# Kernel tuning notes

Hardware: AMD Instinct MI355X
Metric: run time of the kernel (lower is better)

## Reference

```python
import jax, jax.numpy as jnp
import numpy as np

K = 1024   # number of NNLS components (theta_1 is K x K)
B = 8192   # batched frames / columns


def setup_inputs() -> dict:
    key = jax.random.key(0)
    k1, k2, k3, k4 = jax.random.split(key, 4)
    # theta_1 = I - AtA / ||AtA||_F  -> near-identity contraction; emulate with
    # identity minus a small random symmetric-ish perturbation.
    pert = jax.random.normal(k1, (K, K), dtype=jnp.float32) * (1.0 / K)
    th1 = jnp.eye(K, dtype=jnp.float32) - pert
    Y = jax.random.uniform(k2, (K, B), dtype=jnp.float32)
    X_old = jax.random.uniform(k3, (K, B), dtype=jnp.float32)
    weight = jax.random.normal(k4, (K, B), dtype=jnp.float32) * 0.1  # theta_2 = Atb/n_AtA
    k = 2  # PGD iteration counter
    return {"th1": th1, "Y": Y, "X_old": X_old, "k": k, "weight": weight}


def reference(th1, Y, X_old, k, weight):
    # One projected-gradient-descent step of NNLS with Nesterov momentum:
    #   new_X = relu(th1 @ Y + weight)
    #   Y_new = new_X + (k-1)/(k+2) * (new_X - X_old)
    kf = jnp.float32(k)
    new_X = jax.nn.relu(jnp.matmul(th1, Y) + weight)          # [K, B]
    momentum = (kf - 1.0) / (kf + 2.0)
    Y_new = new_X + momentum * (new_X - X_old)                # [K, B]
    return (Y_new, new_X, k + 1, weight)
```

## Files before the change

### kernel.cpp

```cpp
#include <hip/hip_runtime.h>
#include <cstdint>


#define KDIM 1024
#define NDIM 8192
#define KB_ELEMS (1024UL * 8192UL)
#define YT_BYTES (8192UL * 1024UL * 2UL)
#define AB_BYTES (1024UL * 1024UL * 2UL)
#define WS_NEED (YT_BYTES + AB_BYTES)

typedef short short8 __attribute__((ext_vector_type(8)));
typedef float f32x4 __attribute__((ext_vector_type(4)));

struct __attribute__((aligned(4))) f4u { float x, y, z, w; };

__device__ __forceinline__ uint32_t pk2(float a, float b) {
  uint32_t ua = __builtin_bit_cast(uint32_t, a) + 0x8000u;
  uint32_t ub = __builtin_bit_cast(uint32_t, b) + 0x8000u;
  return (ua >> 16) | (ub & 0xFFFF0000u);
}

__device__ __forceinline__ void ldsload16(const void* g, void* l) {
  __builtin_amdgcn_global_load_lds(
      (const __attribute__((address_space(1))) uint32_t*)g,
      (__attribute__((address_space(3))) uint32_t*)l, 16, 0, 0);
}

__global__ __launch_bounds__(256) void nnls_conv(
    const float* __restrict__ th1, const float* __restrict__ Y,
    char* __restrict__ ws)
{
  unsigned short* yt  = (unsigned short*)ws;
  unsigned short* abf = (unsigned short*)(ws + YT_BYTES);
  const int tid = threadIdx.x;
  if (blockIdx.x < 1024) {
    const int kt = blockIdx.x >> 5;
    const int n  = (blockIdx.x & 31) * 256 + tid;
    const float* src = Y + (size_t)kt * 32 * NDIM + n;
    float v[32];
#pragma unroll
    for (int r = 0; r < 32; ++r) v[r] = src[(size_t)r * NDIM];
    __attribute__((aligned(16))) uint32_t o[16];
#pragma unroll
    for (int r = 0; r < 16; ++r) o[r] = pk2(v[2 * r], v[2 * r + 1]);
    const int perm = (n >> 1) & 3;
    uint4* dst = (uint4*)(yt + ((size_t)kt * NDIM + n) * 32);
    const uint4* o4 = (const uint4*)o;
#pragma unroll
    for (int q = 0; q < 4; ++q) dst[q ^ perm] = o4[q];
  } else {
    const int id = (blockIdx.x - 1024) * 256 + tid;
    const int kt = id >> 10, m = id & 1023;
    const float4* s4 = (const float4*)(th1 + (size_t)m * KDIM + kt * 32);
    __attribute__((aligned(16))) uint32_t o[16];
#pragma unroll
    for (int q = 0; q < 8; ++q) {
      const float4 v = s4[q];
      o[2 * q]     = pk2(v.x, v.y);
      o[2 * q + 1] = pk2(v.z, v.w);
    }
    const int perm = (m >> 1) & 3;
    uint4* dst = (uint4*)(abf + ((size_t)kt * KDIM + m) * 32);
    const uint4* o4 = (const uint4*)o;
#pragma unroll
    for (int q = 0; q < 4; ++q) dst[q ^ perm] = o4[q];
  }
}

__global__ __launch_bounds__(128, 2) void nnls_gemm3(
    const char* __restrict__ ws, const float* __restrict__ xold,
    const int* __restrict__ kin, const float* __restrict__ weight,
    float* __restrict__ out)
{
  const char* yt = ws;
  const char* ab = ws + YT_BYTES;
  __shared__ __align__(16) char smem[24576];

  const int tid  = threadIdx.x;
  const int lane = tid & 63;
  const int w    = tid >> 6;
  const int quad = lane >> 4, nl = lane & 15;

  const int m0 = blockIdx.y * 128;
  const int n0 = blockIdx.x * 64;

  const char* ag = ab + (size_t)m0 * 64 + w * 4096 + lane * 16;
  const char* bg = yt + (size_t)n0 * 64 + w * 2048 + lane * 16;

  f32x4 acc[4][4] = {};

  {
#pragma unroll
    for (int q = 0; q < 4; ++q) ldsload16(ag + q * 1024, smem + w * 4096 + q * 1024);
#pragma unroll
    for (int q = 0; q < 2; ++q) ldsload16(bg + q * 1024, smem + 8192 + w * 2048 + q * 1024);
  }
  __syncthreads();

  const int fro = (quad ^ ((nl >> 1) & 3)) * 8;

#pragma unroll 2
  for (int kt = 0; kt < 32; ++kt) {
    char* cur = smem + (kt & 1) * 12288;
    char* nxt = smem + ((kt & 1) ^ 1) * 12288;
    if (kt < 31) {
      const char* a2 = ag + (size_t)(kt + 1) * 65536;
      const char* b2 = bg + (size_t)(kt + 1) * 524288;
#pragma unroll
      for (int q = 0; q < 4; ++q) ldsload16(a2 + q * 1024, nxt + w * 4096 + q * 1024);
#pragma unroll
      for (int q = 0; q < 2; ++q) ldsload16(b2 + q * 1024, nxt + 8192 + w * 2048 + q * 1024);
    }
    const unsigned short* Asp = (const unsigned short*)cur;
    const unsigned short* Bsp = (const unsigned short*)(cur + 8192);
    short8 af[4], bf[4];
#pragma unroll
    for (int i = 0; i < 4; ++i)
      af[i] = *(const short8*)&Asp[(w * 64 + i * 16 + nl) * 32 + fro];
#pragma unroll
    for (int j = 0; j < 4; ++j)
      bf[j] = *(const short8*)&Bsp[(j * 16 + nl) * 32 + fro];
#pragma unroll
    for (int i = 0; i < 4; ++i)
#pragma unroll
      for (int j = 0; j < 4; ++j)
        acc[i][j] = __builtin_amdgcn_mfma_f32_16x16x32_bf16(af[i], bf[j], acc[i][j], 0, 0, 0);
    __syncthreads();
  }

  const float kf  = (float)kin[0];
  const float mom = (kf - 1.0f) / (kf + 2.0f);
  float* ep = (float*)(smem + w * 4608);
  const int u  = lane >> 4;
  const int cq = lane & 15;

#pragma unroll
  for (int i = 0; i < 4; ++i) {
    const int mgb = m0 + w * 64 + i * 16;
    size_t idxs[4]; float4 wv[4], xo[4];
#pragma unroll
    for (int t = 0; t < 4; ++t) {
      idxs[t] = (size_t)(mgb + t * 4 + u) * NDIM + n0 + cq * 4;
      wv[t] = *(const float4*)&weight[idxs[t]];
      xo[t] = *(const float4*)&xold[idxs[t]];
    }
#pragma unroll
    for (int j = 0; j < 4; ++j)
#pragma unroll
      for (int r = 0; r < 4; ++r)
        ep[(quad * 4 + r) * 68 + j * 16 + nl] = acc[i][j][r];
#pragma unroll
    for (int t = 0; t < 4; ++t) {
      const float4 cv = *(const float4*)&ep[(t * 4 + u) * 68 + cq * 4];
      const size_t idx = idxs[t];
      float4 nx, yn;
      nx.x = fmaxf(cv.x + wv[t].x, 0.0f); nx.y = fmaxf(cv.y + wv[t].y, 0.0f);
      nx.z = fmaxf(cv.z + wv[t].z, 0.0f); nx.w = fmaxf(cv.w + wv[t].w, 0.0f);
      yn.x = nx.x + mom * (nx.x - xo[t].x); yn.y = nx.y + mom * (nx.y - xo[t].y);
      yn.z = nx.z + mom * (nx.z - xo[t].z); yn.w = nx.w + mom * (nx.w - xo[t].w);
      *(float4*)&out[idx] = yn;
      *(float4*)&out[KB_ELEMS + idx] = nx;
      f4u s; s.x = wv[t].x; s.y = wv[t].y; s.z = wv[t].z; s.w = wv[t].w;
      *(f4u*)&out[2 * KB_ELEMS + 1 + idx] = s;
    }
  }

  if (blockIdx.x == 0 && blockIdx.y == 0 && tid == 0)
    out[2 * KB_ELEMS] = (float)(kin[0] + 1);
}

#define LDA 40
__global__ __launch_bounds__(512, 4) void nnls_gemm_v1(
    const float* __restrict__ th1, const float* __restrict__ Y,
    const float* __restrict__ xold, const int* __restrict__ kin,
    const float* __restrict__ weight, float* __restrict__ out)
{
  __shared__ __align__(16) char smem[40960];
  unsigned short* As0 = (unsigned short*)smem;
  unsigned short* Bs0 = (unsigned short*)(smem + 10240);
  unsigned short* As1 = (unsigned short*)(smem + 20480);
  unsigned short* Bs1 = (unsigned short*)(smem + 30720);

  const int tid  = threadIdx.x;
  const int lane = tid & 63;
  const int w    = tid >> 6;
  const int wm = w >> 1, wn = w & 1;
  const int quad = lane >> 4, nl = lane & 15;
  const int m0 = blockIdx.y * 128;
  const int n0 = blockIdx.x * 128;
  const int ar = tid >> 3;
  const int ac = tid & 7;
  const float* abase = th1 + (size_t)(m0 + ar) * KDIM + ac * 4;
  const int bn = tid & 127;
  const int bk = (tid >> 7) * 8;
  const float* ybase = Y + (size_t)bk * NDIM + n0 + bn;

  float4 abv[2];
  float  yb[8];
  abv[0] = *(const float4*)(abase);
  abv[1] = *(const float4*)(abase + (size_t)64 * KDIM);
#pragma unroll
  for (int r = 0; r < 8; ++r) yb[r] = ybase[(size_t)r * NDIM];

  f32x4 acc[2][4] = {};

#pragma unroll 2
  for (int kt = 0; kt < 32; ++kt) {
    unsigned short* Asp = (kt & 1) ? As1 : As0;
    unsigned short* Bsp = (kt & 1) ? Bs1 : Bs0;
    {
      uint2 d0; d0.x = pk2(abv[0].x, abv[0].y); d0.y = pk2(abv[0].z, abv[0].w);
      *(uint2*)&Asp[ar * LDA + ac * 4] = d0;
      uint2 d1; d1.x = pk2(abv[1].x, abv[1].y); d1.y = pk2(abv[1].z, abv[1].w);
      *(uint2*)&Asp[(ar + 64) * LDA + ac * 4] = d1;
      uint4 e;
      e.x = pk2(yb[0], yb[1]); e.y = pk2(yb[2], yb[3]);
      e.z = pk2(yb[4], yb[5]); e.w = pk2(yb[6], yb[7]);
      *(uint4*)&Bsp[bn * LDA + bk] = e;
    }
    __syncthreads();
    if (kt < 31) {
      const float* an = abase + (kt + 1) * 32;
      abv[0] = *(const float4*)(an);
      abv[1] = *(const float4*)(an + (size_t)64 * KDIM);
      const float* yn = ybase + (size_t)((kt + 1) * 32) * NDIM;
#pragma unroll
      for (int r = 0; r < 8; ++r) yb[r] = yn[(size_t)r * NDIM];
    }
    short8 af[2], bf[4];
#pragma unroll
    for (int i = 0; i < 2; ++i)
      af[i] = *(const short8*)&Asp[(wm * 32 + i * 16 + nl) * LDA + quad * 8];
#pragma unroll
    for (int j = 0; j < 4; ++j)
      bf[j] = *(const short8*)&Bsp[(wn * 64 + j * 16 + nl) * LDA + quad * 8];
#pragma unroll
    for (int i = 0; i < 2; ++i)
#pragma unroll
      for (int j = 0; j < 4; ++j)
        acc[i][j] = __builtin_amdgcn_mfma_f32_16x16x32_bf16(af[i], bf[j], acc[i][j], 0, 0, 0);
    __syncthreads();
  }
  __syncthreads();

  const float kf  = (float)kin[0];
  const float mom = (kf - 1.0f) / (kf + 2.0f);
  float* ep = (float*)smem + w * 1088;
  const int u  = lane >> 4;
  const int mc = lane & 15;
#pragma unroll
  for (int i = 0; i < 2; ++i) {
#pragma unroll
    for (int j = 0; j < 4; ++j)
#pragma unroll
      for (int r = 0; r < 4; ++r)
        ep[(quad * 4 + r) * 68 + (j * 16 + nl)] = acc[i][j][r];
    const int mgb = m0 + wm * 32 + i * 16;
#pragma unroll
    for (int t = 0; t < 4; ++t) {
      const int row = t * 4 + u;
      const float4 cv = *(const float4*)&ep[row * 68 + mc * 4];
      const int ng = n0 + wn * 64 + mc * 4;
      const size_t idx = (size_t)(mgb + row) * NDIM + ng;
      const float4 wv = *(const float4*)&weight[idx];
      const float4 xo = *(const float4*)&xold[idx];
      float4 nx, yn;
      nx.x = fmaxf(cv.x + wv.x, 0.0f); nx.y = fmaxf(cv.y + wv.y, 0.0f);
      nx.z = fmaxf(cv.z + wv.z, 0.0f); nx.w = fmaxf(cv.w + wv.w, 0.0f);
      yn.x = nx.x + mom * (nx.x - xo.x); yn.y = nx.y + mom * (nx.y - xo.y);
      yn.z = nx.z + mom * (nx.z - xo.z); yn.w = nx.w + mom * (nx.w - xo.w);
      *(float4*)&out[idx] = yn;
      *(float4*)&out[KB_ELEMS + idx] = nx;
      f4u s; s.x = wv.x; s.y = wv.y; s.z = wv.z; s.w = wv.w;
      *(f4u*)&out[2 * KB_ELEMS + 1 + idx] = s;
    }
  }
  if (blockIdx.x == 0 && blockIdx.y == 0 && tid == 0)
    out[2 * KB_ELEMS] = (float)(kin[0] + 1);
}

extern "C" void kernel_launch(void* const* d_in, const int* in_sizes, int n_in,
                              void* d_out, int out_size, void* d_ws, size_t ws_size,
                              hipStream_t stream) {
  const float* th1  = (const float*)d_in[0];
  const float* Y    = (const float*)d_in[1];
  const float* xold = (const float*)d_in[2];
  const int*   kin  = (const int*)d_in[3];
  const float* wgt  = (const float*)d_in[4];
  float* out = (float*)d_out;

  if (d_ws != nullptr && ws_size >= WS_NEED) {
    nnls_conv<<<1152, 256, 0, stream>>>(th1, Y, (char*)d_ws);
    nnls_gemm3<<<dim3(NDIM / 64, KDIM / 128), 128, 0, stream>>>(
        (const char*)d_ws, xold, kin, wgt, out);
  } else {
    nnls_gemm_v1<<<dim3(NDIM / 128, KDIM / 128), 512, 0, stream>>>(
        th1, Y, xold, kin, wgt, out);
  }
}
```

Baseline: 230.3 us.

## Triple-buffer GEMM LDS pipeline with vmcnt waits and widen Y conversion loads

The GEMM main loop moves from double to triple buffering in LDS. Tiles are prefetched two K-steps ahead, and the full __syncthreads per iteration is replaced by a partial s_waitcnt vmcnt plus a single s_barrier, so more global-to-LDS traffic stays in flight while the MFMAs run. The Y transpose/convert kernel now has each thread handle two columns via float2 loads, which halves the block count for that part. In exchange, LDS use rises to 36 KB per block, which may reduce occupancy, and correctness depends on the hand-counted vmcnt value matching the six outstanding loads per stage.

```diff
diff --git a/kernel.cpp b/kernel.cpp
--- a/kernel.cpp
+++ b/kernel.cpp
@@ -33,23 +33,29 @@
   unsigned short* yt  = (unsigned short*)ws;
   unsigned short* abf = (unsigned short*)(ws + YT_BYTES);
   const int tid = threadIdx.x;
-  if (blockIdx.x < 1024) {
-    const int kt = blockIdx.x >> 5;
-    const int n  = (blockIdx.x & 31) * 256 + tid;
+  if (blockIdx.x < 512) {
+    const int kt = blockIdx.x >> 4;
+    const int n  = (blockIdx.x & 15) * 512 + tid * 2;
     const float* src = Y + (size_t)kt * 32 * NDIM + n;
-    float v[32];
-#pragma unroll
-    for (int r = 0; r < 32; ++r) v[r] = src[(size_t)r * NDIM];
-    __attribute__((aligned(16))) uint32_t o[16];
-#pragma unroll
-    for (int r = 0; r < 16; ++r) o[r] = pk2(v[2 * r], v[2 * r + 1]);
+    float2 v[32];
+#pragma unroll
+    for (int r = 0; r < 32; ++r) v[r] = *(const float2*)&src[(size_t)r * NDIM];
+    __attribute__((aligned(16))) uint32_t oA[16], oB[16];
+#pragma unroll
+    for (int r = 0; r < 16; ++r) {
+      oA[r] = pk2(v[2 * r].x, v[2 * r + 1].x);
+      oB[r] = pk2(v[2 * r].y, v[2 * r + 1].y);
+    }
     const int perm = (n >> 1) & 3;
     uint4* dst = (uint4*)(yt + ((size_t)kt * NDIM + n) * 32);
-    const uint4* o4 = (const uint4*)o;
-#pragma unroll
-    for (int q = 0; q < 4; ++q) dst[q ^ perm] = o4[q];
+    const uint4* a4 = (const uint4*)oA;
+    const uint4* b4 = (const uint4*)oB;
+#pragma unroll
+    for (int q = 0; q < 4; ++q) dst[q ^ perm] = a4[q];
+#pragma unroll
+    for (int q = 0; q < 4; ++q) dst[4 + (q ^ perm)] = b4[q];
   } else {
-    const int id = (blockIdx.x - 1024) * 256 + tid;
+    const int id = (blockIdx.x - 512) * 256 + tid;
     const int kt = id >> 10, m = id & 1023;
     const float4* s4 = (const float4*)(th1 + (size_t)m * KDIM + kt * 32);
     __attribute__((aligned(16))) uint32_t o[16];
@@ -67,14 +73,14 @@
   }
 }
 
-__global__ __launch_bounds__(128, 2) void nnls_gemm3(
+__global__ __launch_bounds__(128, 2) void nnls_gemm4(
     const char* __restrict__ ws, const float* __restrict__ xold,
     const int* __restrict__ kin, const float* __restrict__ weight,
     float* __restrict__ out)
 {
   const char* yt = ws;
   const char* ab = ws + YT_BYTES;
-  __shared__ __align__(16) char smem[24576];
+  __shared__ __align__(16) char smem[36864];
 
   const int tid  = threadIdx.x;
   const int lane = tid & 63;
@@ -87,32 +93,31 @@
   const char* ag = ab + (size_t)m0 * 64 + w * 4096 + lane * 16;
   const char* bg = yt + (size_t)n0 * 64 + w * 2048 + lane * 16;
 
+  auto stage = [&](int kt, int buf) {
+    const char* a2 = ag + (size_t)kt * 65536;
+    const char* b2 = bg + (size_t)kt * 524288;
+    char* d = smem + buf * 12288;
+#pragma unroll
+    for (int q = 0; q < 4; ++q) ldsload16(a2 + q * 1024, d + w * 4096 + q * 1024);
+#pragma unroll
+    for (int q = 0; q < 2; ++q) ldsload16(b2 + q * 1024, d + 8192 + w * 2048 + q * 1024);
+  };
+
+  stage(0, 0);
+  stage(1, 1);
+
   f32x4 acc[4][4] = {};
-
-  {
-#pragma unroll
-    for (int q = 0; q < 4; ++q) ldsload16(ag + q * 1024, smem + w * 4096 + q * 1024);
-#pragma unroll
-    for (int q = 0; q < 2; ++q) ldsload16(bg + q * 1024, smem + 8192 + w * 2048 + q * 1024);
-  }
-  __syncthreads();
-
   const int fro = (quad ^ ((nl >> 1) & 3)) * 8;
 
-#pragma unroll 2
+#pragma unroll
   for (int kt = 0; kt < 32; ++kt) {
-    char* cur = smem + (kt & 1) * 12288;
-    char* nxt = smem + ((kt & 1) ^ 1) * 12288;
-    if (kt < 31) {
-      const char* a2 = ag + (size_t)(kt + 1) * 65536;
-      const char* b2 = bg + (size_t)(kt + 1) * 524288;
-#pragma unroll
-      for (int q = 0; q < 4; ++q) ldsload16(a2 + q * 1024, nxt + w * 4096 + q * 1024);
-#pragma unroll
-      for (int q = 0; q < 2; ++q) ldsload16(b2 + q * 1024, nxt + 8192 + w * 2048 + q * 1024);
-    }
-    const unsigned short* Asp = (const unsigned short*)cur;
-    const unsigned short* Bsp = (const unsigned short*)(cur + 8192);
+    if (kt == 31) { asm volatile("s_waitcnt vmcnt(0)" ::: "memory"); }
+    else          { asm volatile("s_waitcnt vmcnt(6)" ::: "memory"); }
+    __builtin_amdgcn_s_barrier();
+    if (kt < 30) stage(kt + 2, (kt + 2) % 3);
+
+    const unsigned short* Asp = (const unsigned short*)(smem + (kt % 3) * 12288);
+    const unsigned short* Bsp = Asp + 4096;
     short8 af[4], bf[4];
 #pragma unroll
     for (int i = 0; i < 4; ++i)
@@ -125,7 +130,6 @@
 #pragma unroll
       for (int j = 0; j < 4; ++j)
         acc[i][j] = __builtin_amdgcn_mfma_f32_16x16x32_bf16(af[i], bf[j], acc[i][j], 0, 0, 0);
-    __syncthreads();
   }
 
   const float kf  = (float)kin[0];
@@ -290,8 +294,8 @@
   float* out = (float*)d_out;
 
   if (d_ws != nullptr && ws_size >= WS_NEED) {
-    nnls_conv<<<1152, 256, 0, stream>>>(th1, Y, (char*)d_ws);
-    nnls_gemm3<<<dim3(NDIM / 64, KDIM / 128), 128, 0, stream>>>(
+    nnls_conv<<<640, 256, 0, stream>>>(th1, Y, (char*)d_ws);
+    nnls_gemm4<<<dim3(NDIM / 64, KDIM / 128), 128, 0, stream>>>(
         (const char*)d_ws, xold, kin, wgt, out);
   } else {
     nnls_gemm_v1<<<dim3(NDIM / 128, KDIM / 128), 512, 0, stream>>>(
```

Result: no change. 233.7 us (+1.5%).
